# Optimization experiments

Measured on AMD Instinct MI355X. Metric: run time of the kernel, lower is better.

The kernel has to match this reference:

```python
import jax, jax.numpy as jnp
import numpy as np

L, B, S, D, H = 3, 2, 2048, 512, 8
HD = D // H
EPS = 1e-5
NEG = -1e9

def setup_inputs() -> dict:
    key = jax.random.key(0)
    ks = jax.random.split(key, 12)
    sc = 1.0 / np.sqrt(D)
    w = lambda k, shape: (jax.random.normal(k, shape, jnp.float32) * sc)
    return {
        'x': jax.random.normal(ks[0], (B, S, D), jnp.float32),
        'mask': jax.random.randint(ks[1], (B, S), 0, 2).astype(jnp.int32),
        'Wp': w(ks[2], (L, D, D)), 'bp': jnp.zeros((L, D), jnp.float32),
        'gamma': jnp.ones((L, D), jnp.float32), 'beta_ln': jnp.zeros((L, D), jnp.float32),
        'Wq': w(ks[3], (L, D, D)), 'bq': jnp.zeros((L, D), jnp.float32),
        'Wk': w(ks[4], (L, D, D)), 'bk': jnp.zeros((L, D), jnp.float32),
        'Wv': w(ks[5], (L, D, D)), 'bv': jnp.zeros((L, D), jnp.float32),
        'Wo': w(ks[6], (L, D, D)), 'bo': jnp.zeros((L, D), jnp.float32),
        'Wout': w(ks[7], (L * D, D)), 'bout': jnp.zeros((D,), jnp.float32),
    }

def reference(x, mask, Wp, bp, gamma, beta_ln, Wq, bq, Wk, bk, Wv, bv, Wo, bo, Wout, bout):
    # per-level input projection: [L,B,S,D]
    xl = jnp.einsum('bsd,lde->lbse', x, Wp) + bp[:, None, None, :]
    # LayerNorm over last dim
    m = xl.mean(-1, keepdims=True)
    v = xl.var(-1, keepdims=True)
    xn = (xl - m) / jnp.sqrt(v + EPS) * gamma[:, None, None, :] + beta_ln[:, None, None, :]
    proj = lambda W, b: (jnp.einsum('lbsd,lde->lbse', xn, W) + b[:, None, None, :]).reshape(L, B, S, H, HD)
    Q, K, V = proj(Wq, bq), proj(Wk, bk), proj(Wv, bv)
    scores = jnp.einsum('lbqhd,lbkhd->lbhqk', Q, K) / np.sqrt(HD).astype(np.float32)
    scores = jnp.where(mask[None, :, None, None, :] == 0, NEG, scores)
    attn = jax.nn.softmax(scores, axis=-1)  # dropout is identity in eval
    attended = jnp.einsum('lbhqk,lbkhd->lbqhd', attn, V).reshape(L, B, S, D)
    lev = jnp.einsum('lbsd,lde->lbse', attended, Wo) + bo[:, None, None, :]  # [L,B,S,D]
    combined = jnp.moveaxis(lev, 0, 2).reshape(B, S, L * D)  # concat levels on last dim
    return combined @ Wout + bout
```

## Files before the change

kernel.cpp:

```cpp
#include <hip/hip_runtime.h>

typedef unsigned short ushort_t;
typedef __attribute__((ext_vector_type(8))) short bf16x8;
typedef __attribute__((ext_vector_type(4))) float f32x4;
typedef __attribute__((ext_vector_type(4))) unsigned int u32x4;
typedef __attribute__((ext_vector_type(2))) unsigned int u32x2;

#define DI static __device__ __forceinline__

DI ushort_t f2bf(float f){
  unsigned u = __builtin_bit_cast(unsigned, f);
  u += 0x7fffu + ((u >> 16) & 1u);
  return (ushort_t)(u >> 16);
}
DI float bf2f(ushort_t h){ unsigned u = ((unsigned)h) << 16; return __builtin_bit_cast(float, u); }

DI unsigned cvt_pk_bf16(float a, float b){
  unsigned r;
  asm("v_cvt_pk_bf16_f32 %0, %1, %2" : "=v"(r) : "v"(a), "v"(b));
  return r;
}

DI float exp2_fast(float x){
  float r;
  asm("v_exp_f32 %0, %1" : "=v"(r) : "v"(x));
  return r;
}

DI void gload_lds16(const void* g, void* l){
  __builtin_amdgcn_global_load_lds((const __attribute__((address_space(1))) void*)g,
                                   (__attribute__((address_space(3))) void*)l, 16, 0, 0);
}

#define CLOG2E 0.18033688011112042f


__global__ __launch_bounds__(256)
void prep_kernel(const float* __restrict__ x, const float* __restrict__ Wo,
                 const float* __restrict__ Wp, const float* __restrict__ Wq,
                 const float* __restrict__ Wk, const float* __restrict__ Wv,
                 const float* __restrict__ Wout,
                 const float* __restrict__ bq, const float* __restrict__ bk,
                 const float* __restrict__ bv, const int* __restrict__ mask,
                 const float* __restrict__ bo, const float* __restrict__ bout,
                 ushort_t* __restrict__ xb, ushort_t* __restrict__ WoB,
                 ushort_t* __restrict__ WpT, ushort_t* __restrict__ WqkvT,
                 ushort_t* __restrict__ WoutT, float* __restrict__ bqkv,
                 ushort_t* __restrict__ mones, ushort_t* __restrict__ mzero,
                 float* __restrict__ zbias, float* __restrict__ bcomb){
  __shared__ float tile[32][33];
  const int bid = blockIdx.x, tid = threadIdx.x;

  auto do_cast = [&](const float* in, ushort_t* out, int i, int n4){
    if (i >= n4) return;
    float4 v = ((const float4*)in)[i];
    ushort_t r0 = f2bf(v.x), r1 = f2bf(v.y), r2 = f2bf(v.z), r3 = f2bf(v.w);
    ushort_t* o = out + (size_t)i * 4;
    o[0] = r0; o[1] = r1; o[2] = r2; o[3] = r3;
  };
  auto do_transpose = [&](const float* src, ushort_t* dst, int R, int C,
                          int bx, int by, float scale){
    int c0 = bx * 32, r0 = by * 32;
    int tx = tid & 31, ty = tid >> 5;
    #pragma unroll
    for (int p = 0; p < 4; ++p)
      tile[ty + p * 8][tx] = src[(size_t)(r0 + ty + p * 8) * C + c0 + tx];
    __syncthreads();
    #pragma unroll
    for (int p = 0; p < 4; ++p){
      int rr = ty + p * 8;
      dst[(size_t)(c0 + rr) * R + r0 + tx] = f2bf(tile[tx][rr] * scale);
    }
  };

  if (bid < 2048){
    do_cast(x, xb, bid * 256 + tid, 524288);
  } else if (bid < 2816){
    do_cast(Wo, WoB, (bid - 2048) * 256 + tid, 196608);
  } else if (bid < 5888){
    int idx = bid - 2816;
    int w = idx / 768, r = idx % 768;
    int zz = r >> 8, t = r & 255;
    int bx = t & 15, by = t >> 4;
    if (w == 0)      do_transpose(Wp + zz * 262144, WpT + zz * 262144, 512, 512, bx, by, 1.0f);
    else if (w == 1) do_transpose(Wq + zz * 262144, WqkvT + (size_t)zz * 786432, 512, 512, bx, by, CLOG2E);
    else if (w == 2) do_transpose(Wk + zz * 262144, WqkvT + 262144 + (size_t)zz * 786432, 512, 512, bx, by, 1.0f);
    else             do_transpose(Wv + zz * 262144, WqkvT + 524288 + (size_t)zz * 786432, 512, 512, bx, by, 1.0f);
  } else if (bid < 6656){
    int t = bid - 5888;
    do_transpose(Wout, WoutT, 1536, 512, t & 15, t >> 4, 1.0f);
  } else if (bid < 6674){
    int i = (bid - 6656) * 256 + tid;
    if (i < 4608){
      int l = i / 1536, j = i % 1536;
      float v = (j < 512) ? bq[l * 512 + j] * CLOG2E
              : (j < 1024 ? bk[l * 512 + j - 512] : bv[l * 512 + j - 1024]);
      bqkv[i] = v;
    }
  } else if (bid < 6690){
    int i = (bid - 6674) * 256 + tid;
    if (i < 4096){
      int mv = mask[i];
      mones[i] = mv ? (ushort_t)0x3F80 : (ushort_t)0;
      mzero[i] = mv ? (ushort_t)0xFFFF : (ushort_t)0;
    }
    if (i < 512) zbias[i] = 0.f;
  } else {
    int wid = tid >> 6, lane = tid & 63;
    int n = (bid - 6690) * 4 + wid;
    float s = 0.f;
    #pragma unroll
    for (int it = 0; it < 24; ++it){
      int k = it * 64 + lane;
      s += bo[k] * Wout[(size_t)k * 512 + n];
    }
    #pragma unroll
    for (int off = 32; off; off >>= 1) s += __shfl_xor(s, off);
    if (lane == 0) bcomb[n] = s + bout[n];
  }
}


template<int BN>
DI void gemm_mainloop(ushort_t* __restrict__ smem,
                      const ushort_t* __restrict__ A, const ushort_t* __restrict__ Bt,
                      int K, int lda, int ldb, int n0, int m0,
                      f32x4 (&acc)[4][BN / 32]){
  constexpr int NB = BN / 32;
  ushort_t* const As = smem;
  ushort_t* const Bs = smem + 128 * 64;
  const int tid = threadIdx.x, wid = tid >> 6, lane = tid & 63;
  const int wr = wid >> 1, wc = wid & 1, lr = lane & 15, lk = lane >> 4;

  for (int k0 = 0; k0 < K; k0 += 64){
    #pragma unroll
    for (int i = 0; i < 4; ++i){
      const int chunk = i * 256 + wid * 64 + lane;
      const int row = chunk >> 3, cc = chunk & 7;
      gload_lds16(A + (size_t)(m0 + row) * lda + (k0 + cc * 8), &As[(i * 256 + wid * 64) * 8]);
    }
    #pragma unroll
    for (int i = 0; i < NB; ++i){
      const int chunk = i * 256 + wid * 64 + lane;
      const int row = chunk >> 3, cc = chunk & 7;
      gload_lds16(Bt + (size_t)(n0 + row) * ldb + (k0 + cc * 8), &Bs[(i * 256 + wid * 64) * 8]);
    }
    __syncthreads();
    bf16x8 af[4][2], bfr[NB][2];
    #pragma unroll
    for (int m = 0; m < 4; ++m){
      af[m][0] = *(const bf16x8*)&As[(wr * 64 + m * 16 + lr) * 64 + lk * 8];
      af[m][1] = *(const bf16x8*)&As[(wr * 64 + m * 16 + lr) * 64 + 32 + lk * 8];
    }
    #pragma unroll
    for (int n = 0; n < NB; ++n){
      bfr[n][0] = *(const bf16x8*)&Bs[(wc * (BN / 2) + n * 16 + lr) * 64 + lk * 8];
      bfr[n][1] = *(const bf16x8*)&Bs[(wc * (BN / 2) + n * 16 + lr) * 64 + 32 + lk * 8];
    }
    #pragma unroll
    for (int m = 0; m < 4; ++m)
      #pragma unroll
      for (int n = 0; n < NB; ++n){
        acc[m][n] = __builtin_amdgcn_mfma_f32_16x16x32_bf16(af[m][0], bfr[n][0], acc[m][n], 0, 0, 0);
        acc[m][n] = __builtin_amdgcn_mfma_f32_16x16x32_bf16(af[m][1], bfr[n][1], acc[m][n], 0, 0, 0);
      }
    __syncthreads();
  }
}

template<int BF16OUT, int BN>
DI void gemm_store(const f32x4 (&acc)[4][BN / 32], const float* __restrict__ bias,
                   void* __restrict__ Cv, int n0, int m0, int ldc){
  constexpr int NB = BN / 32;
  const int tid = threadIdx.x, wid = tid >> 6, lane = tid & 63;
  const int wr = wid >> 1, wc = wid & 1, lr = lane & 15, lk = lane >> 4;
  #pragma unroll
  for (int n = 0; n < NB; ++n){
    const int col = n0 + wc * (BN / 2) + n * 16 + lr;
    const float bv = bias[col];
    #pragma unroll
    for (int m = 0; m < 4; ++m){
      const int row0 = m0 + wr * 64 + m * 16 + lk * 4;
      #pragma unroll
      for (int j = 0; j < 4; ++j){
        const float v = acc[m][n][j] + bv;
        const size_t idx = (size_t)(row0 + j) * ldc + col;
        if (BF16OUT) ((ushort_t*)Cv)[idx] = f2bf(v);
        else         ((float*)Cv)[idx] = v;
      }
    }
  }
}


template<int BF16OUT, int BN, int VT>
__global__ __launch_bounds__(256)
void gemm_bt(const ushort_t* __restrict__ A, const ushort_t* __restrict__ Bt,
             const float* __restrict__ bias, void* __restrict__ Cv,
             int M, int N, int K, int lda, int ldb, int ldc,
             long long sA, long long sB, long long sC, long long sBias,
             ushort_t* __restrict__ VtG, const ushort_t* __restrict__ mzero){
  constexpr int NB = BN / 32;
  __shared__ ushort_t smem[128 * 64 + BN * 64];
  const int gx = gridDim.x, gy = gridDim.y;
  const int nwg = gx * gy * gridDim.z;
  int flat = blockIdx.x + gx * (blockIdx.y + gy * blockIdx.z);
  flat = (flat & 7) * (nwg >> 3) + (flat >> 3);
  const int bxi = flat % gx;
  const int byi = (flat / gx) % gy;
  const int z   = flat / (gx * gy);

  A += (size_t)z * sA; Bt += (size_t)z * sB; bias += (size_t)z * sBias;
  const int n0 = bxi * BN, m0 = byi * 128;
  const int tid = threadIdx.x, wid = tid >> 6, lane = tid & 63;
  const int wr = wid >> 1, wc = wid & 1, lr = lane & 15, lk = lane >> 4;

  f32x4 acc[4][NB] = {};
  gemm_mainloop<BN>(smem, A, Bt, K, lda, ldb, n0, m0, acc);

  if (VT && n0 >= 1024){
    #pragma unroll
    for (int n = 0; n < NB; ++n){
      const int c = wc * (BN / 2) + n * 16 + lr;
      const float bv = bias[n0 + c];
      #pragma unroll
      for (int m = 0; m < 4; ++m){
        const int r0 = wr * 64 + m * 16 + lk * 4;
        u32x2 pk;
        pk[0] = cvt_pk_bf16(acc[m][n][0] + bv, acc[m][n][1] + bv);
        pk[1] = cvt_pk_bf16(acc[m][n][2] + bv, acc[m][n][3] + bv);
        *(u32x2*)&smem[c * 128 + (r0 ^ ((c & 7) << 3))] = pk;
      }
    }
    __syncthreads();
    constexpr int TPC = 256 / BN;
    constexpr int SPT = 128 / TPC;
    const int d_ = tid / TPC;
    const int sq = tid % TPC;
    const int gcol = n0 + d_;
    const int hh = (gcol - 1024) >> 6, dd = gcol & 63;
    const int b_ = m0 >> 11, s0g = m0 & 2047;
    ushort_t* dst = VtG + (((size_t)(z * 2 + b_) * 8 + hh) * 64 + dd) * 2048 + s0g;
    const ushort_t* mz = mzero + b_ * 2048 + s0g;
    #pragma unroll
    for (int it = 0; it < SPT / 8; ++it){
      const int s0 = sq * SPT + it * 8;
      bf16x8 v = *(const bf16x8*)&smem[d_ * 128 + (s0 ^ ((d_ & 7) << 3))];
      const bf16x8 mzv = *(const bf16x8*)&mz[s0];
      v = v & mzv;
      *(bf16x8*)&dst[s0] = v;
    }
    return;
  }

  void* Cz = BF16OUT ? (void*)((ushort_t*)Cv + (size_t)z * sC)
                     : (void*)((float*)Cv + (size_t)z * sC);
  gemm_store<BF16OUT, BN>(acc, bias, Cz, n0, m0, ldc);
}

__global__ __launch_bounds__(256)
void gemm_dual(const ushort_t* __restrict__ WoutT, const ushort_t* __restrict__ WoB,
               const float* __restrict__ zbias, ushort_t* __restrict__ WcombT,
               const ushort_t* __restrict__ xb, const ushort_t* __restrict__ WpT,
               const float* __restrict__ bp, float* __restrict__ xl){
  __shared__ ushort_t smem[128 * 64 + 64 * 64];
  const int bid = blockIdx.x;
  f32x4 acc[4][2] = {};
  if (bid < 96){
    const int bx = bid & 7, by = (bid >> 3) & 3, z = bid >> 5;
    gemm_mainloop<64>(smem, WoutT + z * 512, WoB + (size_t)z * 262144,
                      512, 1536, 512, bx * 64, by * 128, acc);
    gemm_store<1, 64>(acc, zbias, WcombT + (size_t)z * 512, bx * 64, by * 128, 1536);
  } else {
    int b2 = bid - 96;
    b2 = (b2 & 7) * 96 + (b2 >> 3);
    const int bx = b2 % 24, by = b2 / 24;
    gemm_mainloop<64>(smem, xb, WpT, 512, 512, 512, bx * 64, by * 128, acc);
    gemm_store<0, 64>(acc, bp, xl, bx * 64, by * 128, 1536);
  }
}


__global__ __launch_bounds__(256)
void ln_kernel(const float* __restrict__ xl, ushort_t* __restrict__ xn,
               const float* __restrict__ gamma, const float* __restrict__ beta){
  int rid = blockIdx.x * 4 + (threadIdx.x >> 6);
  int lane = threadIdx.x & 63;
  int l = rid >> 12, bs = rid & 4095;
  const float* row = xl + (size_t)bs * 1536 + l * 512;
  ushort_t* orow = xn + (size_t)bs * 1536 + l * 512;
  float4 a = ((const float4*)row)[lane * 2];
  float4 b4 = ((const float4*)row)[lane * 2 + 1];
  float vals[8] = {a.x, a.y, a.z, a.w, b4.x, b4.y, b4.z, b4.w};
  float s = 0.f, ss = 0.f;
  #pragma unroll
  for (int j = 0; j < 8; ++j){ s += vals[j]; ss += vals[j] * vals[j]; }
  #pragma unroll
  for (int off = 32; off; off >>= 1){
    s += __shfl_xor(s, off);
    ss += __shfl_xor(ss, off);
  }
  float mean = s * (1.0f / 512.0f);
  float var = ss * (1.0f / 512.0f) - mean * mean;
  float inv = rsqrtf(var + 1e-5f);
  const float* g = gamma + l * 512 + lane * 8;
  const float* be = beta + l * 512 + lane * 8;
  float4 g0 = ((const float4*)g)[0], g1 = ((const float4*)g)[1];
  float4 be0 = ((const float4*)be)[0], be1 = ((const float4*)be)[1];
  float gs[8] = {g0.x, g0.y, g0.z, g0.w, g1.x, g1.y, g1.z, g1.w};
  float bs8[8] = {be0.x, be0.y, be0.z, be0.w, be1.x, be1.y, be1.z, be1.w};
  bf16x8 r;
  #pragma unroll
  for (int j = 0; j < 8; ++j)
    r[j] = (short)f2bf((vals[j] - mean) * inv * gs[j] + bs8[j]);
  *(bf16x8*)(orow + lane * 8) = r;
}


__global__ __launch_bounds__(256)
void attn_kernel(const ushort_t* __restrict__ qkv, const ushort_t* __restrict__ VtG,
                 const ushort_t* __restrict__ mones, ushort_t* __restrict__ att){
  const int hz = blockIdx.x, qb = blockIdx.y;
  const int h = hz & 7, z = hz >> 3;
  const int l = z >> 1, b = z & 1;
  const size_t base = ((size_t)(l * 4096 + b * 2048)) * 1536;
  const ushort_t* Qb = qkv + base + h * 64;
  const ushort_t* Kb = qkv + base + 512 + h * 64;
  const ushort_t* Vt = VtG + ((size_t)(z * 8 + h) * 64) * 2048;

  __shared__ __attribute__((aligned(16))) ushort_t Ks[2][64 * 64];
  __shared__ __attribute__((aligned(16))) ushort_t Vs[2][64 * 64];

  const int tid = threadIdx.x, wid = tid >> 6, lane = tid & 63;
  const int lr = lane & 15, lk = lane >> 4;
  const int sw = lr & 7;
  const int qrow = qb * 64 + wid * 16 + lr;

  const ushort_t* qp = Qb + (size_t)qrow * 1536 + lk * 8;
  const bf16x8 q0 = *(const bf16x8*)qp;
  const bf16x8 q1 = *(const bf16x8*)(qp + 32);

  const int ch0 = wid * 64 + lane, ch1 = 256 + wid * 64 + lane;
  const int r0_ = ch0 >> 3, c0_ = (ch0 & 7) ^ (r0_ & 7);
  const int r1_ = ch1 >> 3, c1_ = (ch1 & 7) ^ (r1_ & 7);
  const ushort_t* kg0 = Kb + (size_t)r0_ * 1536 + c0_ * 8;
  const ushort_t* kg1 = Kb + (size_t)r1_ * 1536 + c1_ * 8;
  const ushort_t* vg0 = Vt + (size_t)r0_ * 2048 + c0_ * 8;
  const ushort_t* vg1 = Vt + (size_t)r1_ * 2048 + c1_ * 8;
  ushort_t* const kdA0 = &Ks[0][(wid * 64) * 8];
  ushort_t* const kdA1 = &Ks[0][(256 + wid * 64) * 8];
  ushort_t* const kdB0 = &Ks[1][(wid * 64) * 8];
  ushort_t* const kdB1 = &Ks[1][(256 + wid * 64) * 8];
  ushort_t* const vdA0 = &Vs[0][(wid * 64) * 8];
  ushort_t* const vdA1 = &Vs[0][(256 + wid * 64) * 8];
  ushort_t* const vdB0 = &Vs[1][(wid * 64) * 8];
  ushort_t* const vdB1 = &Vs[1][(256 + wid * 64) * 8];

  const ushort_t* const kbA0 = &Ks[0][lr * 64 + (lk ^ sw) * 8];
  const ushort_t* const kbA4 = &Ks[0][lr * 64 + ((lk ^ sw) ^ 4) * 8];
  const ushort_t* const kbB0 = &Ks[1][lr * 64 + (lk ^ sw) * 8];
  const ushort_t* const kbB4 = &Ks[1][lr * 64 + ((lk ^ sw) ^ 4) * 8];
  const ushort_t* const vbA0 = &Vs[0][lr * 64 + (lk ^ sw) * 8];
  const ushort_t* const vbA4 = &Vs[0][lr * 64 + ((lk ^ sw) ^ 4) * 8];
  const ushort_t* const vbB0 = &Vs[1][lr * 64 + (lk ^ sw) * 8];
  const ushort_t* const vbB4 = &Vs[1][lr * 64 + ((lk ^ sw) ^ 4) * 8];

  const ushort_t* pm = mones + b * 2048 + lk * 8;

  f32x4 o[4] = {};
  f32x4 lrun = {0.f, 0.f, 0.f, 0.f};

  gload_lds16(kg0, kdA0); gload_lds16(kg1, kdA1);
  gload_lds16(vg0, vdA0); gload_lds16(vg1, vdA1);
  kg0 += 98304; kg1 += 98304; vg0 += 64; vg1 += 64;
  __syncthreads();

  auto tile_step = [&](const ushort_t* kb0, const ushort_t* kb4,
                       const ushort_t* vb0, const ushort_t* vb4,
                       ushort_t* sk0, ushort_t* sk1, ushort_t* sv0, ushort_t* sv1,
                       bool doStage){
    if (doStage){
      gload_lds16(kg0, sk0); gload_lds16(kg1, sk1);
      gload_lds16(vg0, sv0); gload_lds16(vg1, sv1);
      kg0 += 98304; kg1 += 98304; vg0 += 64; vg1 += 64;
    }
    const bf16x8 mo0 = *(const bf16x8*)pm;
    const bf16x8 mo1 = *(const bf16x8*)(pm + 32);
    pm += 64;

    f32x4 t[4];
    __builtin_amdgcn_s_setprio(1);
    #pragma unroll
    for (int hh = 0; hh < 4; ++hh){
      const bf16x8 kf0 = *(const bf16x8*)(kb0 + hh * 1024);
      const bf16x8 kf1 = *(const bf16x8*)(kb4 + hh * 1024);
      f32x4 tt = {0.f, 0.f, 0.f, 0.f};
      tt = __builtin_amdgcn_mfma_f32_16x16x32_bf16(kf0, q0, tt, 0, 0, 0);
      tt = __builtin_amdgcn_mfma_f32_16x16x32_bf16(kf1, q1, tt, 0, 0, 0);
      t[hh] = tt;
    }
    __builtin_amdgcn_s_setprio(0);

    unsigned a00, a01, a10, a11, a20, a21, a30, a31;
    a00 = cvt_pk_bf16(exp2_fast(t[0][0]), exp2_fast(t[0][1]));
    a01 = cvt_pk_bf16(exp2_fast(t[0][2]), exp2_fast(t[0][3]));
    a10 = cvt_pk_bf16(exp2_fast(t[1][0]), exp2_fast(t[1][1]));
    a11 = cvt_pk_bf16(exp2_fast(t[1][2]), exp2_fast(t[1][3]));
    a20 = cvt_pk_bf16(exp2_fast(t[2][0]), exp2_fast(t[2][1]));
    a21 = cvt_pk_bf16(exp2_fast(t[2][2]), exp2_fast(t[2][3]));
    a30 = cvt_pk_bf16(exp2_fast(t[3][0]), exp2_fast(t[3][1]));
    a31 = cvt_pk_bf16(exp2_fast(t[3][2]), exp2_fast(t[3][3]));
    asm("v_permlane32_swap_b32 %0, %1" : "+v"(a00), "+v"(a10));
    asm("v_permlane32_swap_b32 %0, %1" : "+v"(a01), "+v"(a11));
    asm("v_permlane32_swap_b32 %0, %1" : "+v"(a20), "+v"(a30));
    asm("v_permlane32_swap_b32 %0, %1" : "+v"(a21), "+v"(a31));
    asm("v_permlane16_swap_b32 %0, %1" : "+v"(a00), "+v"(a10));
    asm("v_permlane16_swap_b32 %0, %1" : "+v"(a01), "+v"(a11));
    asm("v_permlane16_swap_b32 %0, %1" : "+v"(a20), "+v"(a30));
    asm("v_permlane16_swap_b32 %0, %1" : "+v"(a21), "+v"(a31));
    const u32x4 f0 = {a00, a01, a10, a11};
    const u32x4 f1 = {a20, a21, a30, a31};
    const bf16x8 pf0 = __builtin_bit_cast(bf16x8, f0);
    const bf16x8 pf1 = __builtin_bit_cast(bf16x8, f1);

    __builtin_amdgcn_s_setprio(1);
    lrun = __builtin_amdgcn_mfma_f32_16x16x32_bf16(pf0, mo0, lrun, 0, 0, 0);
    lrun = __builtin_amdgcn_mfma_f32_16x16x32_bf16(pf1, mo1, lrun, 0, 0, 0);
    #pragma unroll
    for (int n = 0; n < 4; ++n){
      const bf16x8 v0 = *(const bf16x8*)(vb0 + n * 1024);
      const bf16x8 v1 = *(const bf16x8*)(vb4 + n * 1024);
      o[n] = __builtin_amdgcn_mfma_f32_16x16x32_bf16(pf0, v0, o[n], 0, 0, 0);
      o[n] = __builtin_amdgcn_mfma_f32_16x16x32_bf16(pf1, v1, o[n], 0, 0, 0);
    }
    __builtin_amdgcn_s_setprio(0);
    __syncthreads();
  };

  for (int kt2 = 0; kt2 < 32; kt2 += 2){
    tile_step(kbA0, kbA4, vbA0, vbA4, kdB0, kdB1, vdB0, vdB1, true);
    tile_step(kbB0, kbB4, vbB0, vbB4, kdA0, kdA1, vdA0, vdA1, kt2 + 2 < 32);
  }

  float invj[4];
  #pragma unroll
  for (int j = 0; j < 4; ++j) invj[j] = 1.0f / lrun[j];
  const size_t arow0 = (size_t)(b * 2048 + qb * 64 + wid * 16);
  #pragma unroll
  for (int n = 0; n < 4; ++n)
    #pragma unroll
    for (int j = 0; j < 4; ++j)
      att[(arow0 + lk * 4 + j) * 1536 + l * 512 + h * 64 + n * 16 + lr] = f2bf(o[n][j] * invj[j]);
}


extern "C" void kernel_launch(void* const* d_in, const int* in_sizes, int n_in,
                              void* d_out, int out_size, void* d_ws, size_t ws_size,
                              hipStream_t stream){
  const float* x    = (const float*)d_in[0];
  const int*   mask = (const int*)d_in[1];
  const float* Wp   = (const float*)d_in[2];
  const float* bp   = (const float*)d_in[3];
  const float* gamma= (const float*)d_in[4];
  const float* beta = (const float*)d_in[5];
  const float* Wq   = (const float*)d_in[6];
  const float* bq   = (const float*)d_in[7];
  const float* Wk   = (const float*)d_in[8];
  const float* bk   = (const float*)d_in[9];
  const float* Wv   = (const float*)d_in[10];
  const float* bv   = (const float*)d_in[11];
  const float* Wo   = (const float*)d_in[12];
  const float* bo   = (const float*)d_in[13];
  const float* Wout = (const float*)d_in[14];
  const float* bout = (const float*)d_in[15];

  char* ws = (char*)d_ws;
  size_t off = 0;
  auto alloc = [&](size_t bytes){ void* p = ws + off; off += (bytes + 255) & ~(size_t)255; return p; };
  ushort_t* xb    = (ushort_t*)alloc(4096ull * 512 * 2);
  ushort_t* WpT   = (ushort_t*)alloc(1536ull * 512 * 2);
  ushort_t* WqkvT = (ushort_t*)alloc(3ull * 1536 * 512 * 2);
  ushort_t* WoB   = (ushort_t*)alloc(3ull * 512 * 512 * 2);
  ushort_t* WoutT = (ushort_t*)alloc(512ull * 1536 * 2);
  ushort_t* WcombT= (ushort_t*)alloc(512ull * 1536 * 2);
  float*    bqkv  = (float*)alloc(3ull * 1536 * 4);
  float*    zbias = (float*)alloc(512ull * 4);
  float*    bcomb = (float*)alloc(512ull * 4);
  ushort_t* monesB= (ushort_t*)alloc(4096ull * 2);
  ushort_t* mzeroB= (ushort_t*)alloc(4096ull * 2);
  float*    xl    = (float*)alloc(4096ull * 1536 * 4);
  ushort_t* xn    = (ushort_t*)alloc(4096ull * 1536 * 2);
  ushort_t* qkv   = (ushort_t*)alloc(3ull * 4096 * 1536 * 2);
  ushort_t* att   = (ushort_t*)xl;
  ushort_t* VtG   = (ushort_t*)((char*)xl + 12582912);

  prep_kernel<<<6818, 256, 0, stream>>>(x, Wo, Wp, Wq, Wk, Wv, Wout, bq, bk, bv,
                                        mask, bo, bout,
                                        xb, WoB, WpT, WqkvT, WoutT, bqkv,
                                        monesB, mzeroB, zbias, bcomb);

  gemm_dual<<<864, 256, 0, stream>>>(WoutT, WoB, zbias, WcombT, xb, WpT, bp, xl);

  ln_kernel<<<3072, 256, 0, stream>>>(xl, xn, gamma, beta);
  gemm_bt<1, 64, 1><<<dim3(24, 32, 3), 256, 0, stream>>>(xn, WqkvT, bqkv, qkv,
      4096, 1536, 512, 1536, 512, 1536, 512, 786432, 4096ll * 1536, 1536, VtG, mzeroB);
  attn_kernel<<<dim3(48, 32, 1), 256, 0, stream>>>(qkv, VtG, monesB, att);
  gemm_bt<0, 32, 0><<<dim3(16, 32, 1), 256, 0, stream>>>(att, WcombT, bcomb, (float*)d_out,
      4096, 512, 1536, 1536, 1536, 512, 0, 0, 0, 0, nullptr, nullptr);
}
```

Baseline: 186.8 us.

## Compact unmasked keys and values so attention skips masked key tiles

Computes a prefix scan of the key mask to give each kept position a compacted index. K rows are gathered into a dense buffer by a new compact kernel, and V^T is scattered into compacted columns in the QKV GEMM epilogue. Attention then loops only over tiles holding valid keys, roughly halving the work for a random 0/1 mask. The cost is an extra kernel, a scattered per-element V write, and padding and zeroing logic for the tail tiles.

```diff
diff --git a/kernel.cpp b/kernel.cpp
--- a/kernel.cpp
+++ b/kernel.cpp
@@ -46,9 +46,11 @@
                  ushort_t* __restrict__ xb, ushort_t* __restrict__ WoB,
                  ushort_t* __restrict__ WpT, ushort_t* __restrict__ WqkvT,
                  ushort_t* __restrict__ WoutT, float* __restrict__ bqkv,
-                 ushort_t* __restrict__ mones, ushort_t* __restrict__ mzero,
+                 ushort_t* __restrict__ monesC, int* __restrict__ pos,
                  float* __restrict__ zbias, float* __restrict__ bcomb){
   __shared__ float tile[32][33];
+  __shared__ int lds_scan[4];
+  __shared__ int lds_nl;
   const int bid = blockIdx.x, tid = threadIdx.x;
 
   auto do_cast = [&](const float* in, ushort_t* out, int i, int n4){
@@ -97,17 +99,12 @@
               : (j < 1024 ? bk[l * 512 + j - 512] : bv[l * 512 + j - 1024]);
       bqkv[i] = v;
     }
-  } else if (bid < 6690){
+  } else if (bid < 6676){
     int i = (bid - 6674) * 256 + tid;
-    if (i < 4096){
-      int mv = mask[i];
-      mones[i] = mv ? (ushort_t)0x3F80 : (ushort_t)0;
-      mzero[i] = mv ? (ushort_t)0xFFFF : (ushort_t)0;
-    }
     if (i < 512) zbias[i] = 0.f;
-  } else {
+  } else if (bid < 6804){
     int wid = tid >> 6, lane = tid & 63;
-    int n = (bid - 6690) * 4 + wid;
+    int n = (bid - 6676) * 4 + wid;
     float s = 0.f;
     #pragma unroll
     for (int it = 0; it < 24; ++it){
@@ -117,6 +114,65 @@
     #pragma unroll
     for (int off = 32; off; off >>= 1) s += __shfl_xor(s, off);
     if (lane == 0) bcomb[n] = s + bout[n];
+  } else {
+    const int b = bid - 6804;
+    int v[8]; int s8 = 0;
+    #pragma unroll
+    for (int i = 0; i < 8; ++i){ v[i] = mask[b * 2048 + tid * 8 + i] ? 1 : 0; s8 += v[i]; }
+    const int lane = tid & 63, wid2 = tid >> 6;
+    int ws = s8;
+    #pragma unroll
+    for (int off = 1; off < 64; off <<= 1){
+      int t = __shfl_up(ws, off);
+      if (lane >= off) ws += t;
+    }
+    if (lane == 63) lds_scan[wid2] = ws;
+    __syncthreads();
+    int woff = 0;
+    for (int w = 0; w < wid2; ++w) woff += lds_scan[w];
+    int run = woff + ws - s8;
+    #pragma unroll
+    for (int i = 0; i < 8; ++i){ pos[b * 2049 + tid * 8 + i] = run; run += v[i]; }
+    if (tid == 255){ pos[b * 2049 + 2048] = run; lds_nl = run; }
+    __syncthreads();
+    const int nl = lds_nl;
+    #pragma unroll
+    for (int i = 0; i < 8; ++i){
+      int j = tid * 8 + i;
+      monesC[b * 2048 + j] = (j < nl) ? (ushort_t)0x3F80 : (ushort_t)0;
+    }
+  }
+}
+
+
+__global__ __launch_bounds__(256)
+void compact_kernel(const ushort_t* __restrict__ qkv, const int* __restrict__ mask,
+                    const int* __restrict__ pos, ushort_t* __restrict__ KC,
+                    ushort_t* __restrict__ VtG){
+  const int zb = blockIdx.y, l = zb >> 1, b = zb & 1;
+  const int tid = threadIdx.x;
+  if (blockIdx.x < 32){
+    const int s = blockIdx.x * 64 + (tid >> 2);
+    const int c = (tid & 3) * 128;
+    if (mask[b * 2048 + s]){
+      const int p = pos[b * 2049 + s];
+      const ushort_t* src = qkv + ((size_t)(l * 4096 + b * 2048 + s)) * 1536 + 512 + c;
+      ushort_t* dst = KC + ((size_t)zb * 2048 + p) * 512 + c;
+      #pragma unroll
+      for (int i = 0; i < 16; ++i)
+        *(bf16x8*)(dst + i * 8) = *(const bf16x8*)(src + i * 8);
+    }
+  } else {
+    const int nl = pos[b * 2049 + 2048];
+    const int nt2 = ((((nl + 63) >> 6) + 1) & ~1) * 64;
+    const int padShorts = (nt2 - nl) * 512;
+    bf16x8 zz = {};
+    for (int j = tid * 8; j < padShorts; j += 2048)
+      *(bf16x8*)(KC + ((size_t)zb * 2048 + nl) * 512 + j) = zz;
+    for (int rr = tid; rr < 512; rr += 256){
+      ushort_t* row = VtG + (((size_t)zb * 8 + (rr >> 6)) * 64 + (rr & 63)) * 2048;
+      for (int ccol = nl; ccol < nt2; ++ccol) row[ccol] = 0;
+    }
   }
 }
 
@@ -199,7 +255,8 @@
              const float* __restrict__ bias, void* __restrict__ Cv,
              int M, int N, int K, int lda, int ldb, int ldc,
              long long sA, long long sB, long long sC, long long sBias,
-             ushort_t* __restrict__ VtG, const ushort_t* __restrict__ mzero){
+             ushort_t* __restrict__ VtG, const int* __restrict__ mask,
+             const int* __restrict__ pos){
   constexpr int NB = BN / 32;
   __shared__ ushort_t smem[128 * 64 + BN * 64];
   const int gx = gridDim.x, gy = gridDim.y;
@@ -235,20 +292,20 @@
     __syncthreads();
     constexpr int TPC = 256 / BN;
     constexpr int SPT = 128 / TPC;
-    const int d_ = tid / TPC;
-    const int sq = tid % TPC;
+    const int d_ = tid / TPC, sq = tid % TPC;
     const int gcol = n0 + d_;
     const int hh = (gcol - 1024) >> 6, dd = gcol & 63;
     const int b_ = m0 >> 11, s0g = m0 & 2047;
-    ushort_t* dst = VtG + (((size_t)(z * 2 + b_) * 8 + hh) * 64 + dd) * 2048 + s0g;
-    const ushort_t* mz = mzero + b_ * 2048 + s0g;
+    ushort_t* dstrow = VtG + (((size_t)(z * 2 + b_) * 8 + hh) * 64 + dd) * 2048;
+    const int* posb = pos + b_ * 2049 + s0g;
+    const int* mkb  = mask + b_ * 2048 + s0g;
     #pragma unroll
     for (int it = 0; it < SPT / 8; ++it){
       const int s0 = sq * SPT + it * 8;
       bf16x8 v = *(const bf16x8*)&smem[d_ * 128 + (s0 ^ ((d_ & 7) << 3))];
-      const bf16x8 mzv = *(const bf16x8*)&mz[s0];
-      v = v & mzv;
-      *(bf16x8*)&dst[s0] = v;
+      #pragma unroll
+      for (int j = 0; j < 8; ++j)
+        if (mkb[s0 + j]) dstrow[posb[s0 + j]] = (ushort_t)v[j];
     }
     return;
   }
@@ -318,15 +375,19 @@
 
 
 __global__ __launch_bounds__(256)
-void attn_kernel(const ushort_t* __restrict__ qkv, const ushort_t* __restrict__ VtG,
-                 const ushort_t* __restrict__ mones, ushort_t* __restrict__ att){
+void attn_kernel(const ushort_t* __restrict__ qkv, const ushort_t* __restrict__ KC,
+                 const ushort_t* __restrict__ VtG, const ushort_t* __restrict__ mones,
+                 const int* __restrict__ pos, ushort_t* __restrict__ att){
   const int hz = blockIdx.x, qb = blockIdx.y;
   const int h = hz & 7, z = hz >> 3;
   const int l = z >> 1, b = z & 1;
   const size_t base = ((size_t)(l * 4096 + b * 2048)) * 1536;
   const ushort_t* Qb = qkv + base + h * 64;
-  const ushort_t* Kb = qkv + base + 512 + h * 64;
+  const ushort_t* Kb = KC + (size_t)z * 2048 * 512 + h * 64;
   const ushort_t* Vt = VtG + ((size_t)(z * 8 + h) * 64) * 2048;
+
+  const int nl = pos[b * 2049 + 2048];
+  const int nt2 = (((nl + 63) >> 6) + 1) & ~1;
 
   __shared__ __attribute__((aligned(16))) ushort_t Ks[2][64 * 64];
   __shared__ __attribute__((aligned(16))) ushort_t Vs[2][64 * 64];
@@ -343,8 +404,8 @@
   const int ch0 = wid * 64 + lane, ch1 = 256 + wid * 64 + lane;
   const int r0_ = ch0 >> 3, c0_ = (ch0 & 7) ^ (r0_ & 7);
   const int r1_ = ch1 >> 3, c1_ = (ch1 & 7) ^ (r1_ & 7);
-  const ushort_t* kg0 = Kb + (size_t)r0_ * 1536 + c0_ * 8;
-  const ushort_t* kg1 = Kb + (size_t)r1_ * 1536 + c1_ * 8;
+  const ushort_t* kg0 = Kb + (size_t)r0_ * 512 + c0_ * 8;
+  const ushort_t* kg1 = Kb + (size_t)r1_ * 512 + c1_ * 8;
   const ushort_t* vg0 = Vt + (size_t)r0_ * 2048 + c0_ * 8;
   const ushort_t* vg1 = Vt + (size_t)r1_ * 2048 + c1_ * 8;
   ushort_t* const kdA0 = &Ks[0][(wid * 64) * 8];
@@ -372,7 +433,7 @@
 
   gload_lds16(kg0, kdA0); gload_lds16(kg1, kdA1);
   gload_lds16(vg0, vdA0); gload_lds16(vg1, vdA1);
-  kg0 += 98304; kg1 += 98304; vg0 += 64; vg1 += 64;
+  kg0 += 32768; kg1 += 32768; vg0 += 64; vg1 += 64;
   __syncthreads();
 
   auto tile_step = [&](const ushort_t* kb0, const ushort_t* kb4,
@@ -382,7 +443,7 @@
     if (doStage){
       gload_lds16(kg0, sk0); gload_lds16(kg1, sk1);
       gload_lds16(vg0, sv0); gload_lds16(vg1, sv1);
-      kg0 += 98304; kg1 += 98304; vg0 += 64; vg1 += 64;
+      kg0 += 32768; kg1 += 32768; vg0 += 64; vg1 += 64;
     }
     const bf16x8 mo0 = *(const bf16x8*)pm;
     const bf16x8 mo1 = *(const bf16x8*)(pm + 32);
@@ -437,9 +498,9 @@
     __syncthreads();
   };
 
-  for (int kt2 = 0; kt2 < 32; kt2 += 2){
+  for (int kt2 = 0; kt2 < nt2; kt2 += 2){
     tile_step(kbA0, kbA4, vbA0, vbA4, kdB0, kdB1, vdB0, vdB1, true);
-    tile_step(kbB0, kbB4, vbB0, vbB4, kdA0, kdA1, vdA0, vdA1, kt2 + 2 < 32);
+    tile_step(kbB0, kbB4, vbB0, vbB4, kdA0, kdA1, vdA0, vdA1, kt2 + 2 < nt2);
   }
 
   float invj[4];
@@ -486,25 +547,28 @@
   float*    bqkv  = (float*)alloc(3ull * 1536 * 4);
   float*    zbias = (float*)alloc(512ull * 4);
   float*    bcomb = (float*)alloc(512ull * 4);
-  ushort_t* monesB= (ushort_t*)alloc(4096ull * 2);
-  ushort_t* mzeroB= (ushort_t*)alloc(4096ull * 2);
+  ushort_t* monesC= (ushort_t*)alloc(4096ull * 2);
+  int*      pos   = (int*)alloc(2ull * 2049 * 4);
   float*    xl    = (float*)alloc(4096ull * 1536 * 4);
   ushort_t* xn    = (ushort_t*)alloc(4096ull * 1536 * 2);
   ushort_t* qkv   = (ushort_t*)alloc(3ull * 4096 * 1536 * 2);
   ushort_t* att   = (ushort_t*)xl;
   ushort_t* VtG   = (ushort_t*)((char*)xl + 12582912);
-
-  prep_kernel<<<6818, 256, 0, stream>>>(x, Wo, Wp, Wq, Wk, Wv, Wout, bq, bk, bv,
+  ushort_t* KC    = xn;
+
+  prep_kernel<<<6806, 256, 0, stream>>>(x, Wo, Wp, Wq, Wk, Wv, Wout, bq, bk, bv,
                                         mask, bo, bout,
                                         xb, WoB, WpT, WqkvT, WoutT, bqkv,
-                                        monesB, mzeroB, zbias, bcomb);
+                                        monesC, pos, zbias, bcomb);
 
   gemm_dual<<<864, 256, 0, stream>>>(WoutT, WoB, zbias, WcombT, xb, WpT, bp, xl);
 
   ln_kernel<<<3072, 256, 0, stream>>>(xl, xn, gamma, beta);
   gemm_bt<1, 64, 1><<<dim3(24, 32, 3), 256, 0, stream>>>(xn, WqkvT, bqkv, qkv,
-      4096, 1536, 512, 1536, 512, 1536, 512, 786432, 4096ll * 1536, 1536, VtG, mzeroB);
-  attn_kernel<<<dim3(48, 32, 1), 256, 0, stream>>>(qkv, VtG, monesB, att);
+      4096, 1536, 512, 1536, 512, 1536, 512, 786432, 4096ll * 1536, 1536,
+      VtG, mask, pos);
+  compact_kernel<<<dim3(33, 6), 256, 0, stream>>>(qkv, mask, pos, KC, VtG);
+  attn_kernel<<<dim3(48, 32, 1), 256, 0, stream>>>(qkv, KC, VtG, monesC, pos, att);
   gemm_bt<0, 32, 0><<<dim3(16, 32, 1), 256, 0, stream>>>(att, WcombT, bcomb, (float*)d_out,
-      4096, 512, 1536, 1536, 1536, 512, 0, 0, 0, 0, nullptr, nullptr);
-}
+      4096, 512, 1536, 1536, 1536, 512, 0, 0, 0, 0, nullptr, nullptr, nullptr);
+}
```

Measured after the change: 186.8 us. Within noise of the previous version (+0.0%).
